# Performance work log

Hardware: AMD Instinct MI355X
Metric: run time of the kernel (lower is better)

Reference implementation:

```python
import jax, jax.numpy as jnp
import numpy as np

TEMPERATURE = 0.07
EPS = 1e-12  # F.normalize eps

B, D = 4096, 512

def setup_inputs() -> dict:
    key = jax.random.key(0)
    k1, k2, k3 = jax.random.split(key, 3)
    z1 = jax.random.normal(k1, (B, D), dtype=jnp.float32)
    z2 = jax.random.normal(k2, (B, D), dtype=jnp.float32)
    labels = jax.random.randint(k3, (B,), 0, 10)
    return {"z1": z1, "z2": z2, "labels": labels}

def _normalize(x):
    # F.normalize(x, dim=1): x / max(||x||, eps)
    n = jnp.linalg.norm(x, axis=1, keepdims=True)
    return x / jnp.maximum(n, EPS)

def reference(z1, z2, labels):
    z1 = _normalize(z1)
    z2 = _normalize(z2)
    batch_size = z1.shape[0]
    features = jnp.concatenate([z1, z2], axis=0)  # [2B, D], unit-norm rows
    # cosine similarity of unit vectors == dot product
    similarity = jnp.einsum('id,jd->ij', features, features) / TEMPERATURE  # [2B,2B]
    # positive mask: (i, i+B) and (i+B, i)
    idx = jnp.arange(2 * batch_size)
    pos_idx = jnp.where(idx < batch_size, idx + batch_size, idx - batch_size)
    # log-softmax over rows (diagonal NOT masked, matching the original)
    log_prob = similarity - jax.nn.logsumexp(similarity, axis=1, keepdims=True)
    pos_log_prob = log_prob[idx, pos_idx]  # [2B]
    loss = -jnp.sum(pos_log_prob) / (2 * batch_size)
    return loss
```

## Files before the change

kernel.cpp:

```cpp
#include <hip/hip_runtime.h>
#include <hip/hip_bf16.h>

#define BSZ   4096
#define DIM   512
#define NROW  8192
#define NBLK_NORM (BSZ / 4)
#define INV_T 14.285714285714285f

typedef float f32x4 __attribute__((ext_vector_type(4)));

#define GLOAD_LDS16(gp, lp) __builtin_amdgcn_global_load_lds( \
    (const __attribute__((address_space(1))) unsigned int*)(const void*)(gp), \
    (__attribute__((address_space(3))) unsigned int*)(void*)(lp), 16, 0, 0)

__device__ __forceinline__ unsigned pack_fp8x4(float4 v, float s) {
    int w = 0;
    w = __builtin_amdgcn_cvt_pk_fp8_f32(v.x * s, v.y * s, w, false);
    w = __builtin_amdgcn_cvt_pk_fp8_f32(v.z * s, v.w * s, w, true);
    return (unsigned)w;
}

__global__ __launch_bounds__(256) void nt_norm(const float* __restrict__ z1,
                                               const float* __restrict__ z2,
                                               unsigned char* __restrict__ F,
                                               float* __restrict__ posbuf,
                                               float* __restrict__ rowsum) {
    __shared__ float pd[4];
    const int wid  = threadIdx.x >> 6;
    const int lane = threadIdx.x & 63;
    const int row  = blockIdx.x * 4 + wid;

    if (threadIdx.x < 8) rowsum[blockIdx.x * 8 + threadIdx.x] = 0.0f;

    const float4* a4 = (const float4*)(z1 + (size_t)row * DIM);
    const float4* b4 = (const float4*)(z2 + (size_t)row * DIM);
    float4 a0 = a4[lane], a1 = a4[64 + lane];
    float4 b0 = b4[lane], b1 = b4[64 + lane];

    float s1 = a0.x*a0.x + a0.y*a0.y + a0.z*a0.z + a0.w*a0.w
             + a1.x*a1.x + a1.y*a1.y + a1.z*a1.z + a1.w*a1.w;
    float s2 = b0.x*b0.x + b0.y*b0.y + b0.z*b0.z + b0.w*b0.w
             + b1.x*b1.x + b1.y*b1.y + b1.z*b1.z + b1.w*b1.w;
    float d  = a0.x*b0.x + a0.y*b0.y + a0.z*b0.z + a0.w*b0.w
             + a1.x*b1.x + a1.y*b1.y + a1.z*b1.z + a1.w*b1.w;

    #pragma unroll
    for (int off = 32; off; off >>= 1) {
        s1 += __shfl_xor(s1, off);
        s2 += __shfl_xor(s2, off);
        d  += __shfl_xor(d,  off);
    }

    const float inv1 = 1.0f / fmaxf(sqrtf(s1), 1e-12f);
    const float inv2 = 1.0f / fmaxf(sqrtf(s2), 1e-12f);

    unsigned char* F1 = F + (size_t)row * DIM;
    unsigned char* F2 = F + (size_t)(BSZ + row) * DIM;
    *(unsigned*)(F1 + lane * 4)       = pack_fp8x4(a0, inv1);
    *(unsigned*)(F1 + 256 + lane * 4) = pack_fp8x4(a1, inv1);
    *(unsigned*)(F2 + lane * 4)       = pack_fp8x4(b0, inv2);
    *(unsigned*)(F2 + 256 + lane * 4) = pack_fp8x4(b1, inv2);

    if (lane == 0) pd[wid] = d * inv1 * inv2;
    __syncthreads();
    if (threadIdx.x == 0)
        posbuf[blockIdx.x] = pd[0] + pd[1] + pd[2] + pd[3];
}

__device__ __forceinline__ void stage_fp8(const unsigned char* __restrict__ Ag,
                                          const unsigned char* __restrict__ Bg,
                                          unsigned char* Asb, unsigned char* Bsb,
                                          int tid, int wid) {
    #pragma unroll
    for (int ch = 0; ch < 4; ++ch) {
        const int i   = ch * 256 + tid;
        const int rr  = i >> 3;
        const int cb  = (i & 7) * 16;
        const int src = cb ^ ((rr & 7) << 4);
        const int seg = (ch * 256 + wid * 64) * 16;
        GLOAD_LDS16(Ag + (size_t)rr * DIM + src, Asb + seg);
        GLOAD_LDS16(Bg + (size_t)rr * DIM + src, Bsb + seg);
    }
}

__global__ __launch_bounds__(256, 4) void simexp(const unsigned char* __restrict__ F,
                                                 float* __restrict__ rowsum) {
    __shared__ __align__(16) unsigned char As[128 * 128];
    __shared__ __align__(16) unsigned char Bs[128 * 128];

    int L = (blockIdx.x & 7) * 260 + (blockIdx.x >> 3);
    int rem = L, s_r = 0;
    for (; s_r < 8; ++s_r) {
        const int rowsz = 36 + 64 * (7 - s_r);
        if (rem < rowsz) break;
        rem -= rowsz;
    }
    int s_c, lr, lc;
    if (rem < 36) {
        s_c = s_r;
        lr = 0;
        while (rem >= 8 - lr) { rem -= 8 - lr; ++lr; }
        lc = lr + rem;
    } else {
        rem -= 36;
        s_c = s_r + 1 + (rem >> 6);
        const int j = rem & 63;
        lr = j >> 3; lc = j & 7;
    }
    const int r = s_r * 8 + lr;
    const int c = s_c * 8 + lc;

    const int tid  = threadIdx.x;
    const int wid  = tid >> 6;
    const int lane = tid & 63;
    const int wr   = wid >> 1;
    const int wc   = wid & 1;
    const size_t row0 = (size_t)r * 128;
    const size_t col0 = (size_t)c * 128;
    const unsigned char* Abase = F + row0 * DIM;
    const unsigned char* Bbase = F + col0 * DIM;

    f32x4 acc[4][4] = {};

    const int rlo = lane & 15;
    const int g8  = (lane >> 4) * 8;
    const int sw  = (lane & 7) << 4;

    for (int kt = 0; kt < 4; ++kt) {
        stage_fp8(Abase + kt * 128, Bbase + kt * 128, As, Bs, tid, wid);
        __syncthreads();

        #pragma unroll
        for (int ks = 0; ks < 4; ++ks) {
            const int col = (ks * 32 + g8) ^ sw;
            long a[4], b[4];
            #pragma unroll
            for (int n = 0; n < 4; ++n) {
                const int row = wc * 64 + n * 16 + rlo;
                b[n] = *(const long*)(Bs + row * 128 + col);
            }
            #pragma unroll
            for (int m = 0; m < 4; ++m) {
                const int row = wr * 64 + m * 16 + rlo;
                a[m] = *(const long*)(As + row * 128 + col);
            }
            #pragma unroll
            for (int m = 0; m < 4; ++m)
                #pragma unroll
                for (int n = 0; n < 4; ++n)
                    acc[m][n] = __builtin_amdgcn_mfma_f32_16x16x32_fp8_fp8(
                        a[m], b[n], acc[m][n], 0, 0, 0);
        }
        __syncthreads();
    }

    float p[4][4][4];
    #pragma unroll
    for (int m = 0; m < 4; ++m)
        #pragma unroll
        for (int n = 0; n < 4; ++n)
            #pragma unroll
            for (int j = 0; j < 4; ++j)
                p[m][n][j] = __expf((acc[m][n][j] - 1.0f) * INV_T);

    #pragma unroll
    for (int m = 0; m < 4; ++m)
        #pragma unroll
        for (int j = 0; j < 4; ++j) {
            float rs = p[m][0][j] + p[m][1][j] + p[m][2][j] + p[m][3][j];
            rs += __shfl_xor(rs, 1);
            rs += __shfl_xor(rs, 2);
            rs += __shfl_xor(rs, 4);
            rs += __shfl_xor(rs, 8);
            if ((lane & 15) == 0) {
                const int grow = (int)row0 + wr * 64 + m * 16 + ((lane >> 4) << 2) + j;
                atomicAdd(&rowsum[grow], rs);
            }
        }

    if (r != c) {
        #pragma unroll
        for (int n = 0; n < 4; ++n) {
            float cs = 0.f;
            #pragma unroll
            for (int m = 0; m < 4; ++m)
                #pragma unroll
                for (int j = 0; j < 4; ++j)
                    cs += p[m][n][j];
            cs += __shfl_xor(cs, 16);
            cs += __shfl_xor(cs, 32);
            if (lane < 16) {
                const int gcol = (int)col0 + wc * 64 + n * 16 + lane;
                atomicAdd(&rowsum[gcol], cs);
            }
        }
    }
}

__global__ __launch_bounds__(1024) void nt_final(const float* __restrict__ rowsum,
                                                 const float* __restrict__ posbuf,
                                                 float* __restrict__ out) {
    __shared__ float redl[1024];
    __shared__ float redp[1024];
    float s = 0.f, ps = 0.f;
    for (int i = threadIdx.x; i < NROW; i += 1024) s += logf(rowsum[i]);
    for (int i = threadIdx.x; i < NBLK_NORM; i += 1024) ps += posbuf[i];
    redl[threadIdx.x] = s;
    redp[threadIdx.x] = ps;
    __syncthreads();
    for (int off = 512; off; off >>= 1) {
        if (threadIdx.x < off) {
            redl[threadIdx.x] += redl[threadIdx.x + off];
            redp[threadIdx.x] += redp[threadIdx.x + off];
        }
        __syncthreads();
    }
    if (threadIdx.x == 0) {
        out[0] = INV_T + redl[0] / (float)NROW - redp[0] * INV_T / (float)BSZ;
    }
}

extern "C" void kernel_launch(void* const* d_in, const int* in_sizes, int n_in,
                              void* d_out, int out_size, void* d_ws, size_t ws_size,
                              hipStream_t stream) {
    const float* z1 = (const float*)d_in[0];
    const float* z2 = (const float*)d_in[1];

    unsigned char* F = (unsigned char*)d_ws;
    const size_t FBYTES = (size_t)NROW * DIM;
    float* rowsum = (float*)((char*)d_ws + FBYTES);
    float* posbuf = rowsum + NROW;

    nt_norm<<<dim3(NBLK_NORM), dim3(256), 0, stream>>>(z1, z2, F, posbuf, rowsum);
    simexp<<<dim3(2080), dim3(256), 0, stream>>>(F, rowsum);
    nt_final<<<dim3(1), dim3(1024), 0, stream>>>(rowsum, posbuf, (float*)d_out);
}
```

Measured before the change: 52.86 us.

## Compute two column tiles per block with 32x32 fp8 MFMA for A reuse

Each block now computes a 128x256 strip (one A tile against two adjacent B tiles) over the upper triangle, cutting the grid from 2080 to 1056 blocks and reusing the staged A tile across both outputs. The MFMA shape moves from 16x16x32 to 32x32x16 fp8, which needs fewer LDS fragment loads per FLOP. LDS use grows to 48KB per block and occupancy drops to 3 blocks per CU. The odd last strip duplicates a tile and masks out its results.

```diff
diff --git a/kernel.cpp b/kernel.cpp
--- a/kernel.cpp
+++ b/kernel.cpp
@@ -6,8 +6,9 @@
 #define NROW  8192
 #define NBLK_NORM (BSZ / 4)
 #define INV_T 14.285714285714285f
-
-typedef float f32x4 __attribute__((ext_vector_type(4)));
+#define NSTRIP 1056
+
+typedef float f32x16 __attribute__((ext_vector_type(16)));
 
 #define GLOAD_LDS16(gp, lp) __builtin_amdgcn_global_load_lds( \
     (const __attribute__((address_space(1))) unsigned int*)(const void*)(gp), \
@@ -67,132 +68,125 @@
         posbuf[blockIdx.x] = pd[0] + pd[1] + pd[2] + pd[3];
 }
 
-__device__ __forceinline__ void stage_fp8(const unsigned char* __restrict__ Ag,
-                                          const unsigned char* __restrict__ Bg,
-                                          unsigned char* Asb, unsigned char* Bsb,
-                                          int tid, int wid) {
-    #pragma unroll
-    for (int ch = 0; ch < 4; ++ch) {
-        const int i   = ch * 256 + tid;
-        const int rr  = i >> 3;
-        const int cb  = (i & 7) * 16;
-        const int src = cb ^ ((rr & 7) << 4);
-        const int seg = (ch * 256 + wid * 64) * 16;
-        GLOAD_LDS16(Ag + (size_t)rr * DIM + src, Asb + seg);
-        GLOAD_LDS16(Bg + (size_t)rr * DIM + src, Bsb + seg);
-    }
-}
-
-__global__ __launch_bounds__(256, 4) void simexp(const unsigned char* __restrict__ F,
+__global__ __launch_bounds__(256, 3) void simexp(const unsigned char* __restrict__ F,
                                                  float* __restrict__ rowsum) {
     __shared__ __align__(16) unsigned char As[128 * 128];
-    __shared__ __align__(16) unsigned char Bs[128 * 128];
-
-    int L = (blockIdx.x & 7) * 260 + (blockIdx.x >> 3);
-    int rem = L, s_r = 0;
-    for (; s_r < 8; ++s_r) {
-        const int rowsz = 36 + 64 * (7 - s_r);
-        if (rem < rowsz) break;
-        rem -= rowsz;
-    }
-    int s_c, lr, lc;
-    if (rem < 36) {
-        s_c = s_r;
-        lr = 0;
-        while (rem >= 8 - lr) { rem -= 8 - lr; ++lr; }
-        lc = lr + rem;
-    } else {
-        rem -= 36;
-        s_c = s_r + 1 + (rem >> 6);
-        const int j = rem & 63;
-        lr = j >> 3; lc = j & 7;
-    }
-    const int r = s_r * 8 + lr;
-    const int c = s_c * 8 + lc;
+    __shared__ __align__(16) unsigned char Bs[2][128 * 128];
+
+    int L = (blockIdx.x & 7) * 132 + (blockIdx.x >> 3);
+    int r = 0, rem = L;
+    while (true) {
+        const int ns = (65 - r) >> 1;
+        if (rem < ns) break;
+        rem -= ns; ++r;
+    }
+    const int  c0   = r + 2 * rem;
+    const int  c1   = c0 + 1;
+    const bool c1ok = (c1 < 64);
+    const bool diag = (rem == 0);
 
     const int tid  = threadIdx.x;
     const int wid  = tid >> 6;
     const int lane = tid & 63;
     const int wr   = wid >> 1;
     const int wc   = wid & 1;
+    const int l31  = lane & 31;
     const size_t row0 = (size_t)r * 128;
-    const size_t col0 = (size_t)c * 128;
-    const unsigned char* Abase = F + row0 * DIM;
-    const unsigned char* Bbase = F + col0 * DIM;
-
-    f32x4 acc[4][4] = {};
-
-    const int rlo = lane & 15;
-    const int g8  = (lane >> 4) * 8;
+    const unsigned char* Abase  = F + row0 * DIM;
+    const unsigned char* B0base = F + (size_t)c0 * 128 * DIM;
+    const unsigned char* B1base = c1ok ? (B0base + 128 * DIM) : B0base;
+
+    f32x16 acc[2][2][2] = {};
+
+    const int hi8 = (lane >> 5) * 8;
     const int sw  = (lane & 7) << 4;
 
     for (int kt = 0; kt < 4; ++kt) {
-        stage_fp8(Abase + kt * 128, Bbase + kt * 128, As, Bs, tid, wid);
+        #pragma unroll
+        for (int ch = 0; ch < 4; ++ch) {
+            const int i   = ch * 256 + tid;
+            const int rr  = i >> 3;
+            const int cb  = (i & 7) * 16;
+            const int src = cb ^ ((rr & 7) << 4);
+            const int dst = i * 16;
+            const size_t go = (size_t)rr * DIM + kt * 128 + src;
+            GLOAD_LDS16(Abase  + go, As    + dst);
+            GLOAD_LDS16(B0base + go, Bs[0] + dst);
+            GLOAD_LDS16(B1base + go, Bs[1] + dst);
+        }
         __syncthreads();
 
         #pragma unroll
-        for (int ks = 0; ks < 4; ++ks) {
-            const int col = (ks * 32 + g8) ^ sw;
-            long a[4], b[4];
-            #pragma unroll
-            for (int n = 0; n < 4; ++n) {
-                const int row = wc * 64 + n * 16 + rlo;
-                b[n] = *(const long*)(Bs + row * 128 + col);
+        for (int ks = 0; ks < 8; ++ks) {
+            const int col = ((ks * 16) ^ sw) + hi8;
+            long a[2];
+            #pragma unroll
+            for (int m = 0; m < 2; ++m)
+                a[m] = *(const long*)(As + (wr * 64 + m * 32 + l31) * 128 + col);
+            #pragma unroll
+            for (int t = 0; t < 2; ++t) {
+                long b0 = *(const long*)(Bs[t] + (wc * 64 +      l31) * 128 + col);
+                long b1 = *(const long*)(Bs[t] + (wc * 64 + 32 + l31) * 128 + col);
+                #pragma unroll
+                for (int m = 0; m < 2; ++m) {
+                    acc[t][m][0] = __builtin_amdgcn_mfma_f32_32x32x16_fp8_fp8(
+                        a[m], b0, acc[t][m][0], 0, 0, 0);
+                    acc[t][m][1] = __builtin_amdgcn_mfma_f32_32x32x16_fp8_fp8(
+                        a[m], b1, acc[t][m][1], 0, 0, 0);
+                }
             }
-            #pragma unroll
-            for (int m = 0; m < 4; ++m) {
-                const int row = wr * 64 + m * 16 + rlo;
-                a[m] = *(const long*)(As + row * 128 + col);
-            }
-            #pragma unroll
-            for (int m = 0; m < 4; ++m)
+        }
+        __syncthreads();
+    }
+
+    #pragma unroll
+    for (int t = 0; t < 2; ++t)
+        #pragma unroll
+        for (int m = 0; m < 2; ++m)
+            #pragma unroll
+            for (int n = 0; n < 2; ++n)
                 #pragma unroll
-                for (int n = 0; n < 4; ++n)
-                    acc[m][n] = __builtin_amdgcn_mfma_f32_16x16x32_fp8_fp8(
-                        a[m], b[n], acc[m][n], 0, 0, 0);
-        }
-        __syncthreads();
-    }
-
-    float p[4][4][4];
-    #pragma unroll
-    for (int m = 0; m < 4; ++m)
-        #pragma unroll
-        for (int n = 0; n < 4; ++n)
-            #pragma unroll
-            for (int j = 0; j < 4; ++j)
-                p[m][n][j] = __expf((acc[m][n][j] - 1.0f) * INV_T);
-
-    #pragma unroll
-    for (int m = 0; m < 4; ++m)
-        #pragma unroll
-        for (int j = 0; j < 4; ++j) {
-            float rs = p[m][0][j] + p[m][1][j] + p[m][2][j] + p[m][3][j];
-            rs += __shfl_xor(rs, 1);
-            rs += __shfl_xor(rs, 2);
-            rs += __shfl_xor(rs, 4);
-            rs += __shfl_xor(rs, 8);
-            if ((lane & 15) == 0) {
-                const int grow = (int)row0 + wr * 64 + m * 16 + ((lane >> 4) << 2) + j;
-                atomicAdd(&rowsum[grow], rs);
-            }
-        }
-
-    if (r != c) {
-        #pragma unroll
-        for (int n = 0; n < 4; ++n) {
+                for (int e = 0; e < 16; ++e)
+                    acc[t][m][n][e] = __expf((acc[t][m][n][e] - 1.0f) * INV_T);
+
+    #pragma unroll
+    for (int m = 0; m < 2; ++m) {
+        f32x16 rs = acc[0][m][0] + acc[0][m][1];
+        if (c1ok) rs += acc[1][m][0] + acc[1][m][1];
+        #pragma unroll
+        for (int e = 0; e < 16; ++e) {
+            float v = rs[e];
+            v += __shfl_xor(v, 1);
+            v += __shfl_xor(v, 2);
+            v += __shfl_xor(v, 4);
+            v += __shfl_xor(v, 8);
+            v += __shfl_xor(v, 16);
+            rs[e] = v;
+        }
+        if ((lane & 31) == 0) {
+            const int rbase = (int)row0 + wr * 64 + m * 32 + 4 * (lane >> 5);
+            #pragma unroll
+            for (int e = 0; e < 16; ++e)
+                atomicAdd(&rowsum[rbase + (e & 3) + 8 * (e >> 2)], rs[e]);
+        }
+    }
+
+    #pragma unroll
+    for (int t = 0; t < 2; ++t) {
+        const bool want = (t == 0) ? (!diag) : c1ok;
+        if (!want) continue;
+        const int cbase = (t == 0 ? c0 : c1) * 128 + wc * 64;
+        #pragma unroll
+        for (int n = 0; n < 2; ++n) {
             float cs = 0.f;
             #pragma unroll
-            for (int m = 0; m < 4; ++m)
+            for (int m = 0; m < 2; ++m)
                 #pragma unroll
-                for (int j = 0; j < 4; ++j)
-                    cs += p[m][n][j];
-            cs += __shfl_xor(cs, 16);
+                for (int e = 0; e < 16; ++e)
+                    cs += acc[t][m][n][e];
             cs += __shfl_xor(cs, 32);
-            if (lane < 16) {
-                const int gcol = (int)col0 + wc * 64 + n * 16 + lane;
-                atomicAdd(&rowsum[gcol], cs);
-            }
+            if (lane < 32)
+                atomicAdd(&rowsum[cbase + n * 32 + lane], cs);
         }
     }
 }
@@ -232,6 +226,6 @@
     float* posbuf = rowsum + NROW;
 
     nt_norm<<<dim3(NBLK_NORM), dim3(256), 0, stream>>>(z1, z2, F, posbuf, rowsum);
-    simexp<<<dim3(2080), dim3(256), 0, stream>>>(F, rowsum);
+    simexp<<<dim3(NSTRIP), dim3(256), 0, stream>>>(F, rowsum);
     nt_final<<<dim3(1), dim3(1024), 0, stream>>>(rowsum, posbuf, (float*)d_out);
 }
```

Result: slower. 102.7 us (+94.3%).
